# Performance work log

Measured on AMD Instinct MI355X. Metric: run time of the kernel, lower is better.

## Reference

```python
import jax, jax.numpy as jnp
import numpy as np

N, C, P, M = 8, 20, 8732, 16
THRESHOLD, NEG_POS_RATIO, ALPHA = 0.5, 3, 1.0


def cxcy_to_xy(c):
    return jnp.concatenate([c[..., :2] - c[..., 2:] / 2.0, c[..., :2] + c[..., 2:] / 2.0], axis=-1)


def xy_to_cxcy(xy):
    return jnp.concatenate([(xy[..., :2] + xy[..., 2:]) / 2.0, xy[..., 2:] - xy[..., :2]], axis=-1)


def cxcy_to_gcxgcy(cxcy, priors):
    g_cxcy = (cxcy[..., :2] - priors[..., :2]) / (priors[..., 2:] / 10.0)
    g_wh = jnp.log(cxcy[..., 2:] / priors[..., 2:]) * 5.0
    return jnp.concatenate([g_cxcy, g_wh], axis=-1)


def jaccard(a, b):
    # a: (M,4), b: (P,4), boundary coords -> IoU (M,P)
    lo = jnp.maximum(a[:, None, :2], b[None, :, :2])
    hi = jnp.minimum(a[:, None, 2:], b[None, :, 2:])
    inter = jnp.prod(jnp.clip(hi - lo, 0.0), axis=-1)
    area_a = jnp.prod(a[:, 2:] - a[:, :2], axis=-1)
    area_b = jnp.prod(b[:, 2:] - b[:, :2], axis=-1)
    return inter / (area_a[:, None] + area_b[None, :] - inter)


def setup_inputs() -> dict:
    key = jax.random.key(0)
    k1, k2, k3, k4, k5, k6 = jax.random.split(key, 6)
    predicted_locs = jax.random.normal(k1, (N, C, P, 4), jnp.float32)
    predicted_scores = jax.random.normal(k2, (N, C, P, 2), jnp.float32)
    # valid ground-truth boundary boxes (x1<x2, y1<y2) in [0,1]
    ctr = jax.random.uniform(k3, (N, C, M, 2), minval=0.2, maxval=0.8)
    wh = jax.random.uniform(k4, (N, C, M, 2), minval=0.05, maxval=0.3)
    boxes = jnp.concatenate([ctr - wh / 2.0, ctr + wh / 2.0], axis=-1)
    # valid priors in cxcywh (w,h > 0 so log-encoding is finite)
    pctr = jax.random.uniform(k5, (P, 2), minval=0.05, maxval=0.95)
    pwh = jax.random.uniform(k6, (P, 2), minval=0.05, maxval=0.5)
    priors_cxcy = jnp.concatenate([pctr, pwh], axis=-1)
    labels = jnp.ones((N, C, M), jnp.int32)  # binary per-class head: object label = 1
    return {
        "predicted_locs": predicted_locs,
        "predicted_scores": predicted_scores,
        "boxes": boxes,
        "labels": labels,
        "priors_cxcy": priors_cxcy,
    }


def _forward(predicted_locs, predicted_scores, boxes, priors_cxcy, labels):
    n_classes = predicted_scores.shape[1]
    n_priors = predicted_scores.shape[2]
    priors_xy = cxcy_to_xy(priors_cxcy)

    def match(b, lab):
        # b: (M,4) boundary, lab: (M,) int
        ov = jaccard(b, priors_xy)                       # (M,P)
        obj_for_prior = jnp.argmax(ov, axis=0)           # (P,)
        ov_for_prior = jnp.max(ov, axis=0)               # (P,)
        prior_for_obj = jnp.argmax(ov, axis=1)           # (M,)
        # force each object to own its best prior
        obj_for_prior = obj_for_prior.at[prior_for_obj].set(jnp.arange(b.shape[0]))
        ov_for_prior = ov_for_prior.at[prior_for_obj].set(1.0)
        cls = jnp.where(ov_for_prior < THRESHOLD, 0, lab[obj_for_prior])  # (P,)
        tl = cxcy_to_gcxgcy(xy_to_cxcy(b[obj_for_prior]), priors_cxcy)    # (P,4)
        return tl, cls

    true_locs, true_classes = jax.vmap(jax.vmap(match))(boxes, labels)  # (N,C,P,4), (N,C,P)

    pos = true_classes != 0                      # (N,C,P)
    posf = pos.astype(predicted_locs.dtype)
    n_pos_bc = posf.sum(axis=2)                  # (N,C) positives per image per class
    n_pos_c = n_pos_bc.sum(axis=0)               # (C,)

    # localization: mean L1 over positive priors (4 coords each), per class
    l1 = jnp.abs(predicted_locs - true_locs).sum(-1) * posf   # (N,C,P)
    loc_loss_c = l1.sum(axis=(0, 2)) / jnp.maximum(n_pos_c * 4.0, 1.0)

    # per-prior binary cross entropy
    logp = jax.nn.log_softmax(predicted_scores, axis=-1)      # (N,C,P,2)
    ce = -jnp.take_along_axis(logp, true_classes[..., None], axis=-1)[..., 0]  # (N,C,P)
    conf_pos_c = (ce * posf).sum(axis=(0, 2))

    # hard negative mining: sort negatives desc per (image,class) row, keep top 3*n_pos
    ce_neg = jnp.where(pos, 0.0, ce)
    ce_neg_sorted = -jnp.sort(-ce_neg, axis=-1)               # (N,C,P) descending
    n_hard = NEG_POS_RATIO * n_pos_bc                         # (N,C)
    ranks = jnp.arange(n_priors, dtype=n_hard.dtype)
    hard_mask = ranks[None, None, :] < n_hard[..., None]
    conf_hard_c = (ce_neg_sorted * hard_mask).sum(axis=(0, 2))

    safe = jnp.maximum(n_pos_c, 1.0)
    loss_c = jnp.where(
        n_pos_c > 0,
        (conf_pos_c + conf_hard_c + ALPHA * loc_loss_c) / safe,
        0.0,
    ) / n_classes
    return loss_c.sum()


def reference(predicted_locs, predicted_scores, boxes, labels, priors_cxcy):
    return _forward(predicted_locs, predicted_scores, boxes, priors_cxcy, labels)
```

## Files before the change

kernel.cpp:

```cpp
#include <hip/hip_runtime.h>
#include <math.h>

#define NN 8
#define CC 20
#define PP 8732
#define MM 16
#define NPR 3
#define SPLIT 12
#define CH 728
#define ROWS (NN * CC)

__device__ __forceinline__ float fast_rcp(float x) { return __builtin_amdgcn_rcpf(x); }
__device__ __forceinline__ float rfl(float x) {
    return __uint_as_float(__builtin_amdgcn_readfirstlane(__float_as_uint(x)));
}

__device__ __forceinline__ float lse2(float a, float b) {
    float mx = fmaxf(a, b);
    float d  = fabsf(a - b);
    return mx + __logf(1.0f + __expf(-d));
}

#define ABLK 256
__global__ __launch_bounds__(ABLK) void mbox_p1(
    const float* __restrict__ locs, const float* __restrict__ scores,
    const float* __restrict__ boxes, const int* __restrict__ labels,
    const float* __restrict__ priors,
    unsigned char* __restrict__ pk8,
    unsigned long long* __restrict__ partials, float* __restrict__ cstats)
{
    const int row = blockIdx.x / SPLIT;
    const int chunk = blockIdx.x - row * SPLIT;
    const int tid = threadIdx.x, lane = tid & 63, wav = tid >> 6;

    __shared__ float s_bcx[MM], s_bcy[MM], s_bw[MM], s_bh[MM];
    __shared__ unsigned int s_pk[4 * MM];
    __shared__ float s_rf[4 * 3];

    float bx1[MM], by1[MM], bx2[MM], by2[MM], bar[MM];
    unsigned int labm = 0;
    {
        const float* bb = boxes + (size_t)row * MM * 4;
        const int*   lb = labels + (size_t)row * MM;
#pragma unroll
        for (int m = 0; m < MM; m++) {
            float x1 = rfl(bb[m * 4 + 0]), y1 = rfl(bb[m * 4 + 1]);
            float x2 = rfl(bb[m * 4 + 2]), y2 = rfl(bb[m * 4 + 3]);
            bx1[m] = x1; by1[m] = y1; bx2[m] = x2; by2[m] = y2;
            bar[m] = rfl((x2 - x1) * (y2 - y1));
            labm |= (lb[m] != 0 ? 1u : 0u) << m;
        }
        labm = __builtin_amdgcn_readfirstlane(labm);
    }
    if (tid < MM) {
        s_bcx[tid] = (bx1[tid] + bx2[tid]) * 0.5f;
        s_bcy[tid] = (by1[tid] + by2[tid]) * 0.5f;
        s_bw[tid]  = bx2[tid] - bx1[tid];
        s_bh[tid]  = by2[tid] - by1[tid];
    }
    __syncthreads();

    const float4* pri4 = (const float4*)priors;
    const float4* loc4 = (const float4*)(locs + (size_t)row * PP * 4);
    const float2* sc2  = (const float2*)(scores + (size_t)row * PP * 2);
    unsigned char* pk  = pk8 + (size_t)row * PP;

    unsigned int bestk[MM];
#pragma unroll
    for (int m = 0; m < MM; m++) bestk[m] = 0u;
    float l_np = 0.0f, l_l1 = 0.0f, l_cp = 0.0f;
    const int p0 = chunk * CH, p1e = min(p0 + CH, PP);

    float4 pr_next;
    if (p0 + tid < p1e) pr_next = pri4[p0 + tid];
    int it = 0;
    for (int p = p0 + tid; p < p1e; p += ABLK, ++it) {
        float4 pr = pr_next;
        if (p + ABLK < p1e) pr_next = pri4[p + ABLK];
        const unsigned int lowb = ((unsigned int)(7 - it) << 8) | (unsigned int)(255 - tid);
        float hw = pr.z * 0.5f, hh = pr.w * 0.5f;
        float px1 = pr.x - hw, py1 = pr.y - hh;
        float px2 = pr.x + hw, py2 = pr.y + hh;
        float area_b = (px2 - px1) * (py2 - py1);
        unsigned int bovk = 0u;
#pragma unroll
        for (int m = 0; m < MM; m++) {
            float dx = fminf(bx2[m], px2) - fmaxf(bx1[m], px1);
            float dy = fminf(by2[m], py2) - fmaxf(by1[m], py1);
            dx = fmaxf(dx, 0.0f); dy = fmaxf(dy, 0.0f);
            float inter = dx * dy;
            float den = (bar[m] + area_b) - inter;
            float iou = inter * fast_rcp(den);
            unsigned int ib = __float_as_uint(iou);
            unsigned int km = (ib & 0xFFFFFFF0u) | (unsigned int)(15 - m);
            bovk = max(bovk, km);
            unsigned int kp = (ib & 0xFFFFF800u) | lowb;
            bestk[m] = max(bestk[m], kp);
        }
        int bm = 15 - (int)(bovk & 15u);
        bool pos = (bovk >= 0x3F000000u) && (((labm >> bm) & 1u) != 0u);
        pk[p] = (unsigned char)((pos ? 16u : 0u) | (unsigned)bm);
        if (pos) {
            float2 sc = sc2[p];
            float4 pl = loc4[p];
            l_np += 1.0f;
            l_cp += lse2(sc.x, sc.y) - sc.y;
            float tx = (s_bcx[bm] - pr.x) * 10.0f / pr.z;
            float ty = (s_bcy[bm] - pr.y) * 10.0f / pr.w;
            float tw = __logf(s_bw[bm] / pr.z) * 5.0f;
            float th = __logf(s_bh[bm] / pr.w) * 5.0f;
            l_l1 += fabsf(pl.x - tx) + fabsf(pl.y - ty) + fabsf(pl.z - tw) + fabsf(pl.w - th);
        }
    }

#pragma unroll
    for (int m = 0; m < MM; m++) {
        unsigned int key = bestk[m];
#pragma unroll
        for (int off = 32; off; off >>= 1) {
            unsigned int o = __shfl_down(key, off);
            if (o > key) key = o;
        }
        if (lane == 0) s_pk[wav * MM + m] = key;
    }
#pragma unroll
    for (int off = 32; off; off >>= 1) {
        l_np += __shfl_down(l_np, off);
        l_l1 += __shfl_down(l_l1, off);
        l_cp += __shfl_down(l_cp, off);
    }
    if (lane == 0) { s_rf[wav * 3] = l_np; s_rf[wav * 3 + 1] = l_l1; s_rf[wav * 3 + 2] = l_cp; }
    __syncthreads();
    if (tid < MM) {
        unsigned int key = s_pk[tid];
        for (int w = 1; w < 4; w++) {
            unsigned int o = s_pk[w * MM + tid];
            if (o > key) key = o;
        }
        int tw  = 255 - (int)(key & 255u);
        int itw = 7 - (int)((key >> 8) & 7u);
        int pm  = p0 + itw * ABLK + tw;
        partials[((size_t)row * MM + tid) * SPLIT + chunk] =
            ((unsigned long long)(key & 0xFFFFF800u) << 32) |
            (unsigned int)(0x7fffffff - pm);
    }
    if (tid == 0) {
        float np = 0, l1 = 0, cp = 0;
        for (int w = 0; w < 4; w++) { np += s_rf[w * 3]; l1 += s_rf[w * 3 + 1]; cp += s_rf[w * 3 + 2]; }
        float* cs = cstats + ((size_t)row * SPLIT + chunk) * 3;
        cs[0] = np; cs[1] = l1; cs[2] = cp;
    }
}

#define CBLK 1024
#define EPT 9
__global__ __launch_bounds__(CBLK) void mbox_sel(
    const float* __restrict__ locs, const float* __restrict__ scores,
    const float* __restrict__ boxes, const int* __restrict__ labels,
    const float* __restrict__ priors,
    const unsigned char* __restrict__ pk8,
    const unsigned long long* __restrict__ partials,
    const float* __restrict__ cstats, float* __restrict__ rstats)
{
    const int row = blockIdx.x, tid = threadIdx.x, lane = tid & 63, wav = tid >> 6;
    __shared__ float s_bcx[MM], s_bcy[MM], s_bw[MM], s_bh[MM];
    __shared__ int s_lab[MM], s_pfo[MM], s_fp[MM];
    __shared__ float s_fv[MM], s_sum[3];
    __shared__ unsigned int s_hist[256];
    __shared__ unsigned int s_prefix, s_Kr, s_K;
    __shared__ float s_redf[16];
    __shared__ int s_redi[16];

    if (tid < MM) {
        s_fp[tid] = -1;
        const float* b = boxes + ((size_t)row * MM + tid) * 4;
        float x1 = b[0], y1 = b[1], x2 = b[2], y2 = b[3];
        s_bcx[tid] = (x1 + x2) * 0.5f; s_bcy[tid] = (y1 + y2) * 0.5f;
        s_bw[tid] = x2 - x1; s_bh[tid] = y2 - y1;
        s_lab[tid] = labels[row * MM + tid];
        const unsigned long long* pr = partials + ((size_t)row * MM + tid) * SPLIT;
        unsigned long long key = pr[0];
        for (int c = 1; c < SPLIT; c++) { unsigned long long o = pr[c]; if (o > key) key = o; }
        s_pfo[tid] = 0x7fffffff - (int)(unsigned)(key & 0xffffffffull);
    }
    if (tid >= 16 && tid < 19) {
        int j = tid - 16; float s = 0;
        for (int c = 0; c < SPLIT; c++) s += cstats[((size_t)row * SPLIT + c) * 3 + j];
        s_sum[j] = s;
    }
    __syncthreads();

    float d_np = 0, d_l1 = 0, d_cp = 0;
    if (tid < MM) {
        int p = s_pfo[tid];
        bool is_last = true;
        for (int mm = tid + 1; mm < MM; mm++) if (s_pfo[mm] == p) is_last = false;
        if (is_last) {
            const float4 pr = ((const float4*)priors)[p];
            const float4 pl = ((const float4*)(locs + (size_t)row * PP * 4))[p];
            const float2 sc = ((const float2*)(scores + (size_t)row * PP * 2))[p];
            float lse = lse2(sc.x, sc.y);
            unsigned int u = pk8[(size_t)row * PP + p];
            if (u & 16u) {
                int mo = u & 15;
                d_np -= 1.0f; d_cp -= (lse - sc.y);
                float tx = (s_bcx[mo] - pr.x) * 10.0f / pr.z;
                float ty = (s_bcy[mo] - pr.y) * 10.0f / pr.w;
                float tw = __logf(s_bw[mo] / pr.z) * 5.0f;
                float th = __logf(s_bh[mo] / pr.w) * 5.0f;
                d_l1 -= fabsf(pl.x - tx) + fabsf(pl.y - ty) + fabsf(pl.z - tw) + fabsf(pl.w - th);
            }
            if (s_lab[tid] != 0) {
                d_np += 1.0f; d_cp += (lse - sc.y);
                float tx = (s_bcx[tid] - pr.x) * 10.0f / pr.z;
                float ty = (s_bcy[tid] - pr.y) * 10.0f / pr.w;
                float tw = __logf(s_bw[tid] / pr.z) * 5.0f;
                float th = __logf(s_bh[tid] / pr.w) * 5.0f;
                d_l1 += fabsf(pl.x - tx) + fabsf(pl.y - ty) + fabsf(pl.z - tw) + fabsf(pl.w - th);
                s_fv[tid] = 0.0f;
            } else {
                s_fv[tid] = fmaxf(lse - sc.x, 0.0f);
            }
            s_fp[tid] = p;
        }
    }
    if (tid < 64) {
#pragma unroll
        for (int off = 32; off; off >>= 1) {
            d_np += __shfl_down(d_np, off);
            d_l1 += __shfl_down(d_l1, off);
            d_cp += __shfl_down(d_cp, off);
        }
        if (tid == 0) {
            float np = s_sum[0] + d_np;
            rstats[(size_t)row * 8 + 0] = np;
            rstats[(size_t)row * 8 + 1] = s_sum[1] + d_l1;
            rstats[(size_t)row * 8 + 2] = s_sum[2] + d_cp;
            int K = NPR * (int)(np + 0.5f);
            s_K = (K > 0) ? (unsigned)K : 0u;
            s_prefix = 0u;
            s_Kr = (K > 0) ? (unsigned)K : 0u;
        }
    }
    __syncthreads();

    const float2* sc2 = (const float2*)(scores + (size_t)row * PP * 2);
    const unsigned char* pk = pk8 + (size_t)row * PP;
    unsigned int uv[EPT];
#pragma unroll
    for (int k = 0; k < EPT; k++) {
        int p = tid + k * CBLK;
        if (p < PP) {
            unsigned int u8 = pk[p];
            float2 sc = sc2[p];
            float ce = (u8 & 16u) ? 0.0f : fmaxf(lse2(sc.x, sc.y) - sc.x, 0.0f);
            uv[k] = __float_as_uint(ce);
        } else uv[k] = 0u;
    }
    for (int t = 0; t < MM; t++) {
        int fp = s_fp[t];
        if (fp >= 0) {
            unsigned int fb = __float_as_uint(s_fv[t]);
#pragma unroll
            for (int k = 0; k < EPT; k++) if (tid + k * CBLK == fp) uv[k] = fb;
        }
    }

    const unsigned int K = s_K;
    unsigned int T = 0u;
    if (K > 0u && K < PP) {
        for (int pass = 0; pass < 4; pass++) {
            const int shift = 24 - 8 * pass;
            if (tid < 256) s_hist[tid] = 0u;
            __syncthreads();
            const unsigned int pref   = s_prefix;
            const unsigned int maskhi = (pass == 0) ? 0u : (0xffffffffu << (shift + 8));
#pragma unroll
            for (int k = 0; k < EPT; k++) {
                unsigned int u = uv[k];
                if ((u & maskhi) == pref) atomicAdd(&s_hist[(u >> shift) & 255u], 1u);
            }
            __syncthreads();
            if (wav == 0) {
                unsigned int Kr = s_Kr;
                unsigned int h0 = s_hist[lane * 4 + 0];
                unsigned int h1 = s_hist[lane * 4 + 1];
                unsigned int h2 = s_hist[lane * 4 + 2];
                unsigned int h3 = s_hist[lane * 4 + 3];
                unsigned int c3 = h3;
                unsigned int c2 = h3 + h2;
                unsigned int c1 = c2 + h1;
                unsigned int c0 = c1 + h0;
                unsigned int suf = c0;
#pragma unroll
                for (int off = 1; off < 64; off <<= 1) {
                    unsigned int o = __shfl_down(suf, off);
                    if (lane + off < 64) suf += o;
                }
                unsigned int above = suf - c0;
                int cand = -1;
                unsigned int G = 0;
                if      (c3 + above >= Kr) { cand = lane * 4 + 3; G = above + c3 - h3; }
                else if (c2 + above >= Kr) { cand = lane * 4 + 2; G = above + c2 - h2; }
                else if (c1 + above >= Kr) { cand = lane * 4 + 1; G = above + c1 - h1; }
                else if (c0 + above >= Kr) { cand = lane * 4 + 0; G = above + c0 - h0; }
                int best = cand;
#pragma unroll
                for (int off = 32; off; off >>= 1) best = max(best, __shfl_down(best, off));
                best = __shfl(best, 0);
                if (cand == best && cand >= 0) {
                    s_Kr = Kr - G;
                    s_prefix = pref | ((unsigned int)best << shift);
                }
            }
            __syncthreads();
        }
        T = s_prefix;
    }

    float sgt = 0.0f; int cgt = 0;
    if (K > 0u) {
#pragma unroll
        for (int k = 0; k < EPT; k++) {
            unsigned int u = uv[k];
            if (u > T) { sgt += __uint_as_float(u); cgt++; }
        }
    }
#pragma unroll
    for (int off = 32; off; off >>= 1) {
        sgt += __shfl_down(sgt, off);
        cgt += __shfl_down(cgt, off);
    }
    if (lane == 0) { s_redf[wav] = sgt; s_redi[wav] = cgt; }
    __syncthreads();
    if (tid == 0) {
        float s = 0; int cnt = 0;
        for (int w = 0; w < 16; w++) { s += s_redf[w]; cnt += s_redi[w]; }
        float chard = (K > 0u) ? (s + (float)(int)(K - (unsigned)cnt) * __uint_as_float(T)) : 0.0f;
        rstats[(size_t)row * 8 + 4] = chard;
    }
}

__global__ void mbox_finalize(const float* __restrict__ rstats, float* __restrict__ out) {
    int c = threadIdx.x;
    float loss = 0.0f;
    if (c < CC) {
        float np = 0, l1 = 0, cp = 0, ch = 0;
        for (int n = 0; n < NN; n++) {
            const float* s = rstats + ((size_t)(n * CC + c)) * 8;
            np += s[0]; l1 += s[1]; cp += s[2]; ch += s[4];
        }
        float loc = l1 / fmaxf(np * 4.0f, 1.0f);
        float val = (np > 0.0f) ? (cp + ch + loc) / fmaxf(np, 1.0f) : 0.0f;
        loss = val / (float)CC;
    }
#pragma unroll
    for (int off = 32; off; off >>= 1) loss += __shfl_down(loss, off);
    if (threadIdx.x == 0) out[0] = loss;
}

extern "C" void kernel_launch(void* const* d_in, const int* in_sizes, int n_in,
                              void* d_out, int out_size, void* d_ws, size_t ws_size,
                              hipStream_t stream) {
    const float* locs   = (const float*)d_in[0];
    const float* scores = (const float*)d_in[1];
    const float* boxes  = (const float*)d_in[2];
    const int*   labels = (const int*)d_in[3];
    const float* priors = (const float*)d_in[4];
    float* out = (float*)d_out;

    char* ws = (char*)d_ws;
    unsigned char* pk8           = (unsigned char*)ws;
    unsigned long long* partials = (unsigned long long*)(ws + 1397120);
    float* cstats                = (float*)(ws + 1642880);
    float* rstats                = (float*)(ws + 1665920);

    mbox_p1<<<ROWS * SPLIT, ABLK, 0, stream>>>(locs, scores, boxes, labels, priors,
                                               pk8, partials, cstats);
    mbox_sel<<<ROWS, CBLK, 0, stream>>>(locs, scores, boxes, labels, priors,
                                        pk8, partials, cstats, rstats);
    mbox_finalize<<<1, 64, 0, stream>>>(rstats, out);
}
```

Before: 125.6 us.

## Fuse matching pass and hard-negative selection into one per-row kernel

Merges the split matching kernel and the per-row selection kernel into a single 1024-thread block per (image,class) row. Per-prior match codes stay in shared memory and negative CE values stay in registers, so the global pk8/partials/cstats round trip and one launch go away, and scores are loaded once. In exchange only 160 blocks run, where the earlier matching pass used 1920, so the heavy IoU loop has far less parallelism across CUs. It also raises per-thread register pressure from the 16-box arrays plus the 9-element uv array.

```diff
diff --git a/kernel.cpp b/kernel.cpp
--- a/kernel.cpp
+++ b/kernel.cpp
@@ -6,9 +6,9 @@
 #define PP 8732
 #define MM 16
 #define NPR 3
-#define SPLIT 12
-#define CH 728
 #define ROWS (NN * CC)
+#define FBLK 1024
+#define EPT 9
 
 __device__ __forceinline__ float fast_rcp(float x) { return __builtin_amdgcn_rcpf(x); }
 __device__ __forceinline__ float rfl(float x) {
@@ -21,21 +21,23 @@
     return mx + __logf(1.0f + __expf(-d));
 }
 
-#define ABLK 256
-__global__ __launch_bounds__(ABLK) void mbox_p1(
+__global__ __launch_bounds__(FBLK) void mbox_fused(
     const float* __restrict__ locs, const float* __restrict__ scores,
     const float* __restrict__ boxes, const int* __restrict__ labels,
-    const float* __restrict__ priors,
-    unsigned char* __restrict__ pk8,
-    unsigned long long* __restrict__ partials, float* __restrict__ cstats)
+    const float* __restrict__ priors, float* __restrict__ rstats)
 {
-    const int row = blockIdx.x / SPLIT;
-    const int chunk = blockIdx.x - row * SPLIT;
-    const int tid = threadIdx.x, lane = tid & 63, wav = tid >> 6;
-
+    const int row = blockIdx.x, tid = threadIdx.x, lane = tid & 63, wav = tid >> 6;
+
+    __shared__ unsigned char s_pkb[PP];
+    __shared__ unsigned long long s_pk64[16 * MM];
     __shared__ float s_bcx[MM], s_bcy[MM], s_bw[MM], s_bh[MM];
-    __shared__ unsigned int s_pk[4 * MM];
-    __shared__ float s_rf[4 * 3];
+    __shared__ float s_rf[16 * 3];
+    __shared__ int s_lab[MM], s_pfo[MM], s_fp[MM];
+    __shared__ float s_fv[MM];
+    __shared__ unsigned int s_hist[256];
+    __shared__ unsigned int s_prefix, s_Kr, s_K;
+    __shared__ float s_redf[16];
+    __shared__ int s_redi[16];
 
     float bx1[MM], by1[MM], bx2[MM], by2[MM], bar[MM];
     unsigned int labm = 0;
@@ -57,27 +59,31 @@
         s_bcy[tid] = (by1[tid] + by2[tid]) * 0.5f;
         s_bw[tid]  = bx2[tid] - bx1[tid];
         s_bh[tid]  = by2[tid] - by1[tid];
+        s_lab[tid] = labels[row * MM + tid];
+        s_fp[tid]  = -1;
     }
     __syncthreads();
 
     const float4* pri4 = (const float4*)priors;
     const float4* loc4 = (const float4*)(locs + (size_t)row * PP * 4);
     const float2* sc2  = (const float2*)(scores + (size_t)row * PP * 2);
-    unsigned char* pk  = pk8 + (size_t)row * PP;
 
     unsigned int bestk[MM];
 #pragma unroll
     for (int m = 0; m < MM; m++) bestk[m] = 0u;
+    unsigned int uv[EPT];
     float l_np = 0.0f, l_l1 = 0.0f, l_cp = 0.0f;
-    const int p0 = chunk * CH, p1e = min(p0 + CH, PP);
-
-    float4 pr_next;
-    if (p0 + tid < p1e) pr_next = pri4[p0 + tid];
-    int it = 0;
-    for (int p = p0 + tid; p < p1e; p += ABLK, ++it) {
+
+    float4 pr_next = pri4[tid];
+    float2 sc_next = sc2[tid];
+#pragma unroll
+    for (int k = 0; k < EPT; k++) {
+        const int p = tid + k * FBLK;
+        if (p >= PP) { uv[k] = 0u; continue; }
         float4 pr = pr_next;
-        if (p + ABLK < p1e) pr_next = pri4[p + ABLK];
-        const unsigned int lowb = ((unsigned int)(7 - it) << 8) | (unsigned int)(255 - tid);
+        float2 sc = sc_next;
+        if (p + FBLK < PP) { pr_next = pri4[p + FBLK]; sc_next = sc2[p + FBLK]; }
+        const unsigned int lowb = (unsigned int)(8 - k);
         float hw = pr.z * 0.5f, hh = pr.w * 0.5f;
         float px1 = pr.x - hw, py1 = pr.y - hh;
         float px2 = pr.x + hw, py2 = pr.y + hh;
@@ -92,36 +98,41 @@
             float den = (bar[m] + area_b) - inter;
             float iou = inter * fast_rcp(den);
             unsigned int ib = __float_as_uint(iou);
-            unsigned int km = (ib & 0xFFFFFFF0u) | (unsigned int)(15 - m);
-            bovk = max(bovk, km);
-            unsigned int kp = (ib & 0xFFFFF800u) | lowb;
-            bestk[m] = max(bestk[m], kp);
+            bovk     = max(bovk,     (ib & 0xFFFFFFF0u) | (unsigned int)(15 - m));
+            bestk[m] = max(bestk[m], (ib & 0xFFFFFFF0u) | lowb);
         }
         int bm = 15 - (int)(bovk & 15u);
         bool pos = (bovk >= 0x3F000000u) && (((labm >> bm) & 1u) != 0u);
-        pk[p] = (unsigned char)((pos ? 16u : 0u) | (unsigned)bm);
+        s_pkb[p] = (unsigned char)((pos ? 16u : 0u) | (unsigned)bm);
+        float lse = lse2(sc.x, sc.y);
         if (pos) {
-            float2 sc = sc2[p];
             float4 pl = loc4[p];
             l_np += 1.0f;
-            l_cp += lse2(sc.x, sc.y) - sc.y;
+            l_cp += lse - sc.y;
             float tx = (s_bcx[bm] - pr.x) * 10.0f / pr.z;
             float ty = (s_bcy[bm] - pr.y) * 10.0f / pr.w;
             float tw = __logf(s_bw[bm] / pr.z) * 5.0f;
             float th = __logf(s_bh[bm] / pr.w) * 5.0f;
             l_l1 += fabsf(pl.x - tx) + fabsf(pl.y - ty) + fabsf(pl.z - tw) + fabsf(pl.w - th);
+            uv[k] = 0u;
+        } else {
+            uv[k] = __float_as_uint(fmaxf(lse - sc.x, 0.0f));
         }
     }
 
 #pragma unroll
     for (int m = 0; m < MM; m++) {
-        unsigned int key = bestk[m];
+        unsigned int bk = bestk[m];
+        int kk = 8 - (int)(bk & 0xFu);
+        int pb = tid + kk * FBLK;
+        unsigned long long key = ((unsigned long long)(bk & 0xFFFFFFF0u) << 32)
+                               | (unsigned int)(0x7fffffff - pb);
 #pragma unroll
         for (int off = 32; off; off >>= 1) {
-            unsigned int o = __shfl_down(key, off);
+            unsigned long long o = __shfl_down(key, off);
             if (o > key) key = o;
         }
-        if (lane == 0) s_pk[wav * MM + m] = key;
+        if (lane == 0) s_pk64[wav * MM + m] = key;
     }
 #pragma unroll
     for (int off = 32; off; off >>= 1) {
@@ -131,62 +142,14 @@
     }
     if (lane == 0) { s_rf[wav * 3] = l_np; s_rf[wav * 3 + 1] = l_l1; s_rf[wav * 3 + 2] = l_cp; }
     __syncthreads();
+
     if (tid < MM) {
-        unsigned int key = s_pk[tid];
-        for (int w = 1; w < 4; w++) {
-            unsigned int o = s_pk[w * MM + tid];
+        unsigned long long key = s_pk64[tid];
+        for (int w = 1; w < 16; w++) {
+            unsigned long long o = s_pk64[w * MM + tid];
             if (o > key) key = o;
         }
-        int tw  = 255 - (int)(key & 255u);
-        int itw = 7 - (int)((key >> 8) & 7u);
-        int pm  = p0 + itw * ABLK + tw;
-        partials[((size_t)row * MM + tid) * SPLIT + chunk] =
-            ((unsigned long long)(key & 0xFFFFF800u) << 32) |
-            (unsigned int)(0x7fffffff - pm);
-    }
-    if (tid == 0) {
-        float np = 0, l1 = 0, cp = 0;
-        for (int w = 0; w < 4; w++) { np += s_rf[w * 3]; l1 += s_rf[w * 3 + 1]; cp += s_rf[w * 3 + 2]; }
-        float* cs = cstats + ((size_t)row * SPLIT + chunk) * 3;
-        cs[0] = np; cs[1] = l1; cs[2] = cp;
-    }
-}
-
-#define CBLK 1024
-#define EPT 9
-__global__ __launch_bounds__(CBLK) void mbox_sel(
-    const float* __restrict__ locs, const float* __restrict__ scores,
-    const float* __restrict__ boxes, const int* __restrict__ labels,
-    const float* __restrict__ priors,
-    const unsigned char* __restrict__ pk8,
-    const unsigned long long* __restrict__ partials,
-    const float* __restrict__ cstats, float* __restrict__ rstats)
-{
-    const int row = blockIdx.x, tid = threadIdx.x, lane = tid & 63, wav = tid >> 6;
-    __shared__ float s_bcx[MM], s_bcy[MM], s_bw[MM], s_bh[MM];
-    __shared__ int s_lab[MM], s_pfo[MM], s_fp[MM];
-    __shared__ float s_fv[MM], s_sum[3];
-    __shared__ unsigned int s_hist[256];
-    __shared__ unsigned int s_prefix, s_Kr, s_K;
-    __shared__ float s_redf[16];
-    __shared__ int s_redi[16];
-
-    if (tid < MM) {
-        s_fp[tid] = -1;
-        const float* b = boxes + ((size_t)row * MM + tid) * 4;
-        float x1 = b[0], y1 = b[1], x2 = b[2], y2 = b[3];
-        s_bcx[tid] = (x1 + x2) * 0.5f; s_bcy[tid] = (y1 + y2) * 0.5f;
-        s_bw[tid] = x2 - x1; s_bh[tid] = y2 - y1;
-        s_lab[tid] = labels[row * MM + tid];
-        const unsigned long long* pr = partials + ((size_t)row * MM + tid) * SPLIT;
-        unsigned long long key = pr[0];
-        for (int c = 1; c < SPLIT; c++) { unsigned long long o = pr[c]; if (o > key) key = o; }
         s_pfo[tid] = 0x7fffffff - (int)(unsigned)(key & 0xffffffffull);
-    }
-    if (tid >= 16 && tid < 19) {
-        int j = tid - 16; float s = 0;
-        for (int c = 0; c < SPLIT; c++) s += cstats[((size_t)row * SPLIT + c) * 3 + j];
-        s_sum[j] = s;
     }
     __syncthreads();
 
@@ -197,10 +160,10 @@
         for (int mm = tid + 1; mm < MM; mm++) if (s_pfo[mm] == p) is_last = false;
         if (is_last) {
             const float4 pr = ((const float4*)priors)[p];
-            const float4 pl = ((const float4*)(locs + (size_t)row * PP * 4))[p];
-            const float2 sc = ((const float2*)(scores + (size_t)row * PP * 2))[p];
+            const float4 pl = loc4[p];
+            const float2 sc = sc2[p];
             float lse = lse2(sc.x, sc.y);
-            unsigned int u = pk8[(size_t)row * PP + p];
+            unsigned int u = s_pkb[p];
             if (u & 16u) {
                 int mo = u & 15;
                 d_np -= 1.0f; d_cp -= (lse - sc.y);
@@ -232,10 +195,14 @@
             d_cp += __shfl_down(d_cp, off);
         }
         if (tid == 0) {
-            float np = s_sum[0] + d_np;
+            float np0 = 0, l10 = 0, cp0 = 0;
+            for (int w = 0; w < 16; w++) {
+                np0 += s_rf[w * 3]; l10 += s_rf[w * 3 + 1]; cp0 += s_rf[w * 3 + 2];
+            }
+            float np = np0 + d_np;
             rstats[(size_t)row * 8 + 0] = np;
-            rstats[(size_t)row * 8 + 1] = s_sum[1] + d_l1;
-            rstats[(size_t)row * 8 + 2] = s_sum[2] + d_cp;
+            rstats[(size_t)row * 8 + 1] = l10 + d_l1;
+            rstats[(size_t)row * 8 + 2] = cp0 + d_cp;
             int K = NPR * (int)(np + 0.5f);
             s_K = (K > 0) ? (unsigned)K : 0u;
             s_prefix = 0u;
@@ -244,25 +211,12 @@
     }
     __syncthreads();
 
-    const float2* sc2 = (const float2*)(scores + (size_t)row * PP * 2);
-    const unsigned char* pk = pk8 + (size_t)row * PP;
-    unsigned int uv[EPT];
-#pragma unroll
-    for (int k = 0; k < EPT; k++) {
-        int p = tid + k * CBLK;
-        if (p < PP) {
-            unsigned int u8 = pk[p];
-            float2 sc = sc2[p];
-            float ce = (u8 & 16u) ? 0.0f : fmaxf(lse2(sc.x, sc.y) - sc.x, 0.0f);
-            uv[k] = __float_as_uint(ce);
-        } else uv[k] = 0u;
-    }
     for (int t = 0; t < MM; t++) {
         int fp = s_fp[t];
         if (fp >= 0) {
             unsigned int fb = __float_as_uint(s_fv[t]);
 #pragma unroll
-            for (int k = 0; k < EPT; k++) if (tid + k * CBLK == fp) uv[k] = fb;
+            for (int k = 0; k < EPT; k++) if (tid + k * FBLK == fp) uv[k] = fb;
         }
     }
 
@@ -369,15 +323,8 @@
     const float* priors = (const float*)d_in[4];
     float* out = (float*)d_out;
 
-    char* ws = (char*)d_ws;
-    unsigned char* pk8           = (unsigned char*)ws;
-    unsigned long long* partials = (unsigned long long*)(ws + 1397120);
-    float* cstats                = (float*)(ws + 1642880);
-    float* rstats                = (float*)(ws + 1665920);
-
-    mbox_p1<<<ROWS * SPLIT, ABLK, 0, stream>>>(locs, scores, boxes, labels, priors,
-                                               pk8, partials, cstats);
-    mbox_sel<<<ROWS, CBLK, 0, stream>>>(locs, scores, boxes, labels, priors,
-                                        pk8, partials, cstats, rstats);
+    float* rstats = (float*)d_ws;
+
+    mbox_fused<<<ROWS, FBLK, 0, stream>>>(locs, scores, boxes, labels, priors, rstats);
     mbox_finalize<<<1, 64, 0, stream>>>(rstats, out);
 }
```

After: 188.9 us. 1.5x slower.

## Compute negative CE in matching pass and stage it in LDS for selection

Applied to the files above, without the earlier changes.

The first kernel now computes the per-prior negative cross-entropy for every prior, prefetching scores alongside priors, and writes it to a float workspace buffer. The selection kernel loads this buffer into a shared-memory array of about 35KB instead of recomputing CE from scores and match flags. The forced-match fixups are written directly into shared memory, which removes the per-thread search loop. In exchange, the first kernel does extra global writes and exp/log work for all priors, and the larger shared-memory footprint may limit occupancy in the 160-block selection kernel.

```diff
diff --git a/kernel.cpp b/kernel.cpp
--- a/kernel.cpp
+++ b/kernel.cpp
@@ -6,9 +6,14 @@
 #define PP 8732
 #define MM 16
 #define NPR 3
+#define ROWS (NN * CC)
+
 #define SPLIT 12
 #define CH 728
-#define ROWS (NN * CC)
+#define ABLK 256
+
+#define FBLK 1024
+#define EPT 9
 
 __device__ __forceinline__ float fast_rcp(float x) { return __builtin_amdgcn_rcpf(x); }
 __device__ __forceinline__ float rfl(float x) {
@@ -21,12 +26,11 @@
     return mx + __logf(1.0f + __expf(-d));
 }
 
-#define ABLK 256
 __global__ __launch_bounds__(ABLK) void mbox_p1(
     const float* __restrict__ locs, const float* __restrict__ scores,
     const float* __restrict__ boxes, const int* __restrict__ labels,
     const float* __restrict__ priors,
-    unsigned char* __restrict__ pk8,
+    float* __restrict__ cef, unsigned char* __restrict__ pk8,
     unsigned long long* __restrict__ partials, float* __restrict__ cstats)
 {
     const int row = blockIdx.x / SPLIT;
@@ -64,6 +68,7 @@
     const float4* loc4 = (const float4*)(locs + (size_t)row * PP * 4);
     const float2* sc2  = (const float2*)(scores + (size_t)row * PP * 2);
     unsigned char* pk  = pk8 + (size_t)row * PP;
+    float* cefr        = cef + (size_t)row * PP;
 
     unsigned int bestk[MM];
 #pragma unroll
@@ -71,12 +76,13 @@
     float l_np = 0.0f, l_l1 = 0.0f, l_cp = 0.0f;
     const int p0 = chunk * CH, p1e = min(p0 + CH, PP);
 
-    float4 pr_next;
-    if (p0 + tid < p1e) pr_next = pri4[p0 + tid];
+    float4 pr_next; float2 sc_next;
+    if (p0 + tid < p1e) { pr_next = pri4[p0 + tid]; sc_next = sc2[p0 + tid]; }
     int it = 0;
     for (int p = p0 + tid; p < p1e; p += ABLK, ++it) {
         float4 pr = pr_next;
-        if (p + ABLK < p1e) pr_next = pri4[p + ABLK];
+        float2 sc = sc_next;
+        if (p + ABLK < p1e) { pr_next = pri4[p + ABLK]; sc_next = sc2[p + ABLK]; }
         const unsigned int lowb = ((unsigned int)(7 - it) << 8) | (unsigned int)(255 - tid);
         float hw = pr.z * 0.5f, hh = pr.w * 0.5f;
         float px1 = pr.x - hw, py1 = pr.y - hh;
@@ -100,17 +106,22 @@
         int bm = 15 - (int)(bovk & 15u);
         bool pos = (bovk >= 0x3F000000u) && (((labm >> bm) & 1u) != 0u);
         pk[p] = (unsigned char)((pos ? 16u : 0u) | (unsigned)bm);
+        float lse = lse2(sc.x, sc.y);
+        float ce;
         if (pos) {
-            float2 sc = sc2[p];
             float4 pl = loc4[p];
             l_np += 1.0f;
-            l_cp += lse2(sc.x, sc.y) - sc.y;
+            l_cp += lse - sc.y;
             float tx = (s_bcx[bm] - pr.x) * 10.0f / pr.z;
             float ty = (s_bcy[bm] - pr.y) * 10.0f / pr.w;
             float tw = __logf(s_bw[bm] / pr.z) * 5.0f;
             float th = __logf(s_bh[bm] / pr.w) * 5.0f;
             l_l1 += fabsf(pl.x - tx) + fabsf(pl.y - ty) + fabsf(pl.z - tw) + fabsf(pl.w - th);
-        }
+            ce = 0.0f;
+        } else {
+            ce = fmaxf(lse - sc.x, 0.0f);
+        }
+        cefr[p] = ce;
     }
 
 #pragma unroll
@@ -152,27 +163,26 @@
     }
 }
 
-#define CBLK 1024
-#define EPT 9
-__global__ __launch_bounds__(CBLK) void mbox_sel(
+__global__ __launch_bounds__(FBLK) void mbox_sel(
     const float* __restrict__ locs, const float* __restrict__ scores,
     const float* __restrict__ boxes, const int* __restrict__ labels,
     const float* __restrict__ priors,
-    const unsigned char* __restrict__ pk8,
+    const float* __restrict__ cef, const unsigned char* __restrict__ pk8,
     const unsigned long long* __restrict__ partials,
     const float* __restrict__ cstats, float* __restrict__ rstats)
 {
     const int row = blockIdx.x, tid = threadIdx.x, lane = tid & 63, wav = tid >> 6;
+
+    __shared__ unsigned int s_u32[PP];
     __shared__ float s_bcx[MM], s_bcy[MM], s_bw[MM], s_bh[MM];
-    __shared__ int s_lab[MM], s_pfo[MM], s_fp[MM];
-    __shared__ float s_fv[MM], s_sum[3];
+    __shared__ int s_lab[MM], s_pfo[MM];
+    __shared__ float s_sum[3];
     __shared__ unsigned int s_hist[256];
     __shared__ unsigned int s_prefix, s_Kr, s_K;
     __shared__ float s_redf[16];
     __shared__ int s_redi[16];
 
     if (tid < MM) {
-        s_fp[tid] = -1;
         const float* b = boxes + ((size_t)row * MM + tid) * 4;
         float x1 = b[0], y1 = b[1], x2 = b[2], y2 = b[3];
         s_bcx[tid] = (x1 + x2) * 0.5f; s_bcy[tid] = (y1 + y2) * 0.5f;
@@ -188,8 +198,15 @@
         for (int c = 0; c < SPLIT; c++) s += cstats[((size_t)row * SPLIT + c) * 3 + j];
         s_sum[j] = s;
     }
-    __syncthreads();
-
+#pragma unroll
+    for (int k = 0; k < EPT; k++) {
+        const int p = tid + k * FBLK;
+        if (p < PP) s_u32[p] = __float_as_uint(cef[(size_t)row * PP + p]);
+    }
+    __syncthreads();
+
+    const float4* loc4 = (const float4*)(locs + (size_t)row * PP * 4);
+    const float2* sc2  = (const float2*)(scores + (size_t)row * PP * 2);
     float d_np = 0, d_l1 = 0, d_cp = 0;
     if (tid < MM) {
         int p = s_pfo[tid];
@@ -197,8 +214,8 @@
         for (int mm = tid + 1; mm < MM; mm++) if (s_pfo[mm] == p) is_last = false;
         if (is_last) {
             const float4 pr = ((const float4*)priors)[p];
-            const float4 pl = ((const float4*)(locs + (size_t)row * PP * 4))[p];
-            const float2 sc = ((const float2*)(scores + (size_t)row * PP * 2))[p];
+            const float4 pl = loc4[p];
+            const float2 sc = sc2[p];
             float lse = lse2(sc.x, sc.y);
             unsigned int u = pk8[(size_t)row * PP + p];
             if (u & 16u) {
@@ -217,11 +234,10 @@
                 float tw = __logf(s_bw[tid] / pr.z) * 5.0f;
                 float th = __logf(s_bh[tid] / pr.w) * 5.0f;
                 d_l1 += fabsf(pl.x - tx) + fabsf(pl.y - ty) + fabsf(pl.z - tw) + fabsf(pl.w - th);
-                s_fv[tid] = 0.0f;
+                s_u32[p] = 0u;
             } else {
-                s_fv[tid] = fmaxf(lse - sc.x, 0.0f);
+                s_u32[p] = __float_as_uint(fmaxf(lse - sc.x, 0.0f));
             }
-            s_fp[tid] = p;
         }
     }
     if (tid < 64) {
@@ -244,28 +260,6 @@
     }
     __syncthreads();
 
-    const float2* sc2 = (const float2*)(scores + (size_t)row * PP * 2);
-    const unsigned char* pk = pk8 + (size_t)row * PP;
-    unsigned int uv[EPT];
-#pragma unroll
-    for (int k = 0; k < EPT; k++) {
-        int p = tid + k * CBLK;
-        if (p < PP) {
-            unsigned int u8 = pk[p];
-            float2 sc = sc2[p];
-            float ce = (u8 & 16u) ? 0.0f : fmaxf(lse2(sc.x, sc.y) - sc.x, 0.0f);
-            uv[k] = __float_as_uint(ce);
-        } else uv[k] = 0u;
-    }
-    for (int t = 0; t < MM; t++) {
-        int fp = s_fp[t];
-        if (fp >= 0) {
-            unsigned int fb = __float_as_uint(s_fv[t]);
-#pragma unroll
-            for (int k = 0; k < EPT; k++) if (tid + k * CBLK == fp) uv[k] = fb;
-        }
-    }
-
     const unsigned int K = s_K;
     unsigned int T = 0u;
     if (K > 0u && K < PP) {
@@ -277,7 +271,8 @@
             const unsigned int maskhi = (pass == 0) ? 0u : (0xffffffffu << (shift + 8));
 #pragma unroll
             for (int k = 0; k < EPT; k++) {
-                unsigned int u = uv[k];
+                const int p = tid + k * FBLK;
+                unsigned int u = (p < PP) ? s_u32[p] : 0u;
                 if ((u & maskhi) == pref) atomicAdd(&s_hist[(u >> shift) & 255u], 1u);
             }
             __syncthreads();
@@ -322,7 +317,8 @@
     if (K > 0u) {
 #pragma unroll
         for (int k = 0; k < EPT; k++) {
-            unsigned int u = uv[k];
+            const int p = tid + k * FBLK;
+            unsigned int u = (p < PP) ? s_u32[p] : 0u;
             if (u > T) { sgt += __uint_as_float(u); cgt++; }
         }
     }
@@ -370,14 +366,15 @@
     float* out = (float*)d_out;
 
     char* ws = (char*)d_ws;
-    unsigned char* pk8           = (unsigned char*)ws;
-    unsigned long long* partials = (unsigned long long*)(ws + 1397120);
-    float* cstats                = (float*)(ws + 1642880);
-    float* rstats                = (float*)(ws + 1665920);
+    float* cef                   = (float*)ws;
+    unsigned char* pk8           = (unsigned char*)(ws + 5588480);
+    unsigned long long* partials = (unsigned long long*)(ws + 6985600);
+    float* cstats                = (float*)(ws + 7231360);
+    float* rstats                = (float*)(ws + 7254400);
 
     mbox_p1<<<ROWS * SPLIT, ABLK, 0, stream>>>(locs, scores, boxes, labels, priors,
-                                               pk8, partials, cstats);
-    mbox_sel<<<ROWS, CBLK, 0, stream>>>(locs, scores, boxes, labels, priors,
-                                        pk8, partials, cstats, rstats);
+                                               cef, pk8, partials, cstats);
+    mbox_sel<<<ROWS, FBLK, 0, stream>>>(locs, scores, boxes, labels, priors,
+                                        cef, pk8, partials, cstats, rstats);
     mbox_finalize<<<1, 64, 0, stream>>>(rstats, out);
 }
```

After: 121.6 us. 3.2% less time.
